# Kernel tuning notes

Hardware: AMD Instinct MI355X
Metric: run time of the kernel (lower is better)

## Reference

```python
import jax, jax.numpy as jnp
import numpy as np

B, S, H, F = 4, 2048, 1024, 4096
E, K = 8, 2


def setup_inputs() -> dict:
    key = jax.random.key(0)
    ks = jax.random.split(key, 8)
    s1 = 1.0 / np.sqrt(H)
    s2 = 1.0 / np.sqrt(F)
    return {
        "hidden_states": jax.random.normal(ks[0], (B, S, H), dtype=jnp.float32),
        "w1": jax.random.normal(ks[1], (E, H, F), dtype=jnp.float32) * s1,
        "b1": jnp.zeros((E, F), dtype=jnp.float32),
        "w2": jax.random.normal(ks[2], (E, F, H), dtype=jnp.float32) * s2,
        "b2": jnp.zeros((E, H), dtype=jnp.float32),
        "router_w": jax.random.normal(ks[3], (H, E), dtype=jnp.float32) * s1,
        "router_b": jnp.zeros((E,), dtype=jnp.float32),
    }


def reference(hidden_states, w1, b1, w2, b2, router_w, router_b):
    b, s, h = hidden_states.shape
    x = hidden_states.reshape(-1, h)              # [T, H]
    # --- router: softmax over expert logits, top-k, renormalize ---
    logits = x @ router_w + router_b              # [T, E]
    probs = jax.nn.softmax(logits, axis=-1)
    top_w, top_i = jax.lax.top_k(probs, K)        # [T, K]
    top_w = top_w / jnp.sum(top_w, axis=-1, keepdims=True)
    # --- dispatch/combine: per-expert FFN, weighted sum (same math as
    # gather/scatter loop in the torch module, expressed densely per expert) ---
    out = jnp.zeros_like(x)
    for e in range(E):
        we = jnp.sum(jnp.where(top_i == e, top_w, 0.0), axis=-1)   # [T]
        he = jax.nn.gelu(x @ w1[e] + b1[e]) @ w2[e] + b2[e]        # [T, H]
        out = out + we[:, None] * he
    return out.reshape(b, s, h)
```

## Files before the change

kernel.cpp:

```cpp
#include <hip/hip_runtime.h>
#include <cstdint>
#include <cstddef>

#define T_TOK 8192
#define HD 1024
#define FD 4096
#define NE 8
#define RCAP 17408

typedef __bf16 bf16_t;
typedef __bf16 bf16x8 __attribute__((ext_vector_type(8)));
typedef __bf16 bf16x4 __attribute__((ext_vector_type(4)));
typedef float floatx4 __attribute__((ext_vector_type(4)));

#define BM 128
#define BN 128
#define BK 64
#define LDS_STRIDE 72

__device__ __forceinline__ float gelu_tanh(float x) {
    float x3 = x * x * x;
    float t = tanhf(0.7978845608028654f * (x + 0.044715f * x3));
    return 0.5f * x * (1.0f + t);
}

__global__ __launch_bounds__(256) void transpose_conv_kernel(
    const float* __restrict__ in, bf16_t* __restrict__ out, int R, int C)
{
    __shared__ float tile[32][33];
    const int e = blockIdx.z;
    const int c0 = blockIdx.x * 32;
    const int r0 = blockIdx.y * 32;
    const float* src = in + (size_t)e * R * C;
    bf16_t* dst = out + (size_t)e * R * C;
    const int tx = threadIdx.x & 31;
    const int ty = threadIdx.x >> 5;
    #pragma unroll
    for (int i = ty; i < 32; i += 8)
        tile[i][tx] = src[(size_t)(r0 + i) * C + c0 + tx];
    __syncthreads();
    #pragma unroll
    for (int i = ty; i < 32; i += 8)
        dst[(size_t)(c0 + i) * R + r0 + tx] = (bf16_t)tile[tx][i];
}

__global__ __launch_bounds__(256) void router_kernel(
    const float* __restrict__ x, const float* __restrict__ rw,
    const float* __restrict__ rb,
    int* __restrict__ tok_e, float* __restrict__ tok_w, int* __restrict__ counts)
{
    const int t = blockIdx.x * 4 + (threadIdx.x >> 6);
    const int lane = threadIdx.x & 63;
    const float* xr = x + (size_t)t * HD;
    float acc[NE];
    #pragma unroll
    for (int e = 0; e < NE; ++e) acc[e] = 0.f;
    #pragma unroll 4
    for (int i = 0; i < HD / 64; ++i) {
        int h = lane + 64 * i;
        float xv = xr[h];
        const float4* w4 = (const float4*)(rw + (size_t)h * NE);
        float4 wa = w4[0], wb = w4[1];
        acc[0] += xv * wa.x; acc[1] += xv * wa.y;
        acc[2] += xv * wa.z; acc[3] += xv * wa.w;
        acc[4] += xv * wb.x; acc[5] += xv * wb.y;
        acc[6] += xv * wb.z; acc[7] += xv * wb.w;
    }
    #pragma unroll
    for (int s = 32; s > 0; s >>= 1)
        #pragma unroll
        for (int e = 0; e < NE; ++e)
            acc[e] += __shfl_xor(acc[e], s, 64);
    if (lane == 0) {
        float l[NE];
        #pragma unroll
        for (int e = 0; e < NE; ++e) l[e] = acc[e] + rb[e];
        int e1 = 0;
        #pragma unroll
        for (int e = 1; e < NE; ++e) if (l[e] > l[e1]) e1 = e;
        int e2 = (e1 == 0) ? 1 : 0;
        #pragma unroll
        for (int e = 0; e < NE; ++e) {
            if (e == e1 || e == e2) continue;
            if (l[e] > l[e2]) e2 = e;
        }
        float m = l[e1];
        float q1 = 1.0f;
        float q2 = expf(l[e2] - m);
        float inv = 1.0f / (q1 + q2);
        tok_e[t * 2]     = e1;
        tok_e[t * 2 + 1] = e2;
        tok_w[t * 2]     = q1 * inv;
        tok_w[t * 2 + 1] = q2 * inv;
        atomicAdd(&counts[e1], 1);
        atomicAdd(&counts[e2], 1);
    }
}

__global__ void offsets_kernel(const int* __restrict__ counts,
                               int* __restrict__ offsets, int* __restrict__ cursors)
{
    if (threadIdx.x == 0) {
        int cum = 0;
        for (int e = 0; e < NE; ++e) {
            offsets[e] = cum;
            cursors[e] = cum;
            cum += (counts[e] + BM - 1) & ~(BM - 1);
        }
    }
}

__global__ __launch_bounds__(256) void gather_kernel(
    const float* __restrict__ x, const int* __restrict__ tok_e,
    const float* __restrict__ tok_w, int* __restrict__ cursors,
    bf16_t* __restrict__ Xg, int* __restrict__ rows_token, float* __restrict__ rows_w)
{
    const int pair = blockIdx.x * 4 + (threadIdx.x >> 6);
    const int lane = threadIdx.x & 63;
    const int t = pair >> 1;
    int pos;
    if (lane == 0) {
        int e = tok_e[pair];
        pos = atomicAdd(&cursors[e], 1);
        rows_token[pos] = t;
        rows_w[pos] = tok_w[pair];
    }
    pos = __shfl(pos, 0, 64);
    const float4* src = (const float4*)(x + (size_t)t * HD);
    bf16_t* dst = Xg + (size_t)pos * HD;
    #pragma unroll
    for (int i = 0; i < HD / 256; ++i) {
        float4 v = src[lane + 64 * i];
        int base = (lane + 64 * i) * 4;
        bf16x4 o;
        o[0] = (bf16_t)v.x; o[1] = (bf16_t)v.y;
        o[2] = (bf16_t)v.z; o[3] = (bf16_t)v.w;
        *(bf16x4*)(dst + base) = o;
    }
}

template<int KDIM>
__device__ __forceinline__ void gemm_tile(
    const bf16_t* __restrict__ aG,
    const bf16_t* __restrict__ bG,
    bf16_t As[BM][LDS_STRIDE], bf16_t Bs[BN][LDS_STRIDE],
    floatx4 acc[4][4])
{
    const int tid = threadIdx.x;
    const int lane = tid & 63;
    const int wave = tid >> 6;
    const int quad = lane >> 4;
    const int l16 = lane & 15;
    const int wm = (wave & 1) * 64;
    const int wn = (wave >> 1) * 64;
    const int r0 = tid >> 3;
    const int c0 = (tid & 7) * 8;

    for (int k0 = 0; k0 < KDIM; k0 += BK) {
        #pragma unroll
        for (int p = 0; p < 4; ++p) {
            int r = p * 32 + r0;
            *(bf16x8*)(&As[r][c0]) = *(const bf16x8*)(aG + (size_t)r * KDIM + k0 + c0);
            *(bf16x8*)(&Bs[r][c0]) = *(const bf16x8*)(bG + (size_t)r * KDIM + k0 + c0);
        }
        __syncthreads();
        #pragma unroll
        for (int kk = 0; kk < BK; kk += 32) {
            bf16x8 af[4], bfr[4];
            #pragma unroll
            for (int i = 0; i < 4; ++i)
                af[i] = *(const bf16x8*)(&As[wm + i * 16 + l16][kk + quad * 8]);
            #pragma unroll
            for (int i = 0; i < 4; ++i)
                bfr[i] = *(const bf16x8*)(&Bs[wn + i * 16 + l16][kk + quad * 8]);
            #pragma unroll
            for (int i = 0; i < 4; ++i)
                #pragma unroll
                for (int j = 0; j < 4; ++j)
                    acc[i][j] = __builtin_amdgcn_mfma_f32_16x16x32_bf16(
                        af[i], bfr[j], acc[i][j], 0, 0, 0);
        }
        __syncthreads();
    }
}

__global__ __launch_bounds__(256) void ffn1_kernel(
    const bf16_t* __restrict__ Xg, const bf16_t* __restrict__ w1t,
    const float* __restrict__ b1, bf16_t* __restrict__ Hb,
    const int* __restrict__ counts, const int* __restrict__ offsets)
{
    const int e = blockIdx.z;
    const int cnt = counts[e];
    const int mtile = blockIdx.y;
    if (mtile * BM >= cnt) return;
    const int m_base = offsets[e] + mtile * BM;
    const int n_base = blockIdx.x * BN;

    __shared__ bf16_t As[BM][LDS_STRIDE];
    __shared__ bf16_t Bs[BN][LDS_STRIDE];
    floatx4 acc[4][4] = {};

    gemm_tile<HD>(Xg + (size_t)m_base * HD,
                  w1t + ((size_t)e * FD + n_base) * HD, As, Bs, acc);

    const int lane = threadIdx.x & 63;
    const int wave = threadIdx.x >> 6;
    const int quad = lane >> 4;
    const int l16 = lane & 15;
    const int wm = (wave & 1) * 64;
    const int wn = (wave >> 1) * 64;
    #pragma unroll
    for (int i = 0; i < 4; ++i) {
        int rl = wm + i * 16 + quad * 4;
        #pragma unroll
        for (int j = 0; j < 4; ++j) {
            int col = n_base + wn + j * 16 + l16;
            float bias = b1[e * FD + col];
            #pragma unroll
            for (int r = 0; r < 4; ++r) {
                float v = acc[i][j][r] + bias;
                Hb[(size_t)(m_base + rl + r) * FD + col] = (bf16_t)gelu_tanh(v);
            }
        }
    }
}

__global__ __launch_bounds__(256) void ffn2_kernel(
    const bf16_t* __restrict__ Hb, const bf16_t* __restrict__ w2t,
    const float* __restrict__ b2, float* __restrict__ out,
    const int* __restrict__ counts, const int* __restrict__ offsets,
    const int* __restrict__ rows_token, const float* __restrict__ rows_w)
{
    const int e = blockIdx.z;
    const int cnt = counts[e];
    const int mtile = blockIdx.y;
    if (mtile * BM >= cnt) return;
    const int m_base = offsets[e] + mtile * BM;
    const int n_base = blockIdx.x * BN;

    __shared__ bf16_t As[BM][LDS_STRIDE];
    __shared__ bf16_t Bs[BN][LDS_STRIDE];
    floatx4 acc[4][4] = {};

    gemm_tile<FD>(Hb + (size_t)m_base * FD,
                  w2t + ((size_t)e * HD + n_base) * FD, As, Bs, acc);

    const int lane = threadIdx.x & 63;
    const int wave = threadIdx.x >> 6;
    const int quad = lane >> 4;
    const int l16 = lane & 15;
    const int wm = (wave & 1) * 64;
    const int wn = (wave >> 1) * 64;
    const int loc_base = mtile * BM;
    #pragma unroll
    for (int i = 0; i < 4; ++i) {
        int rl = wm + i * 16 + quad * 4;
        #pragma unroll
        for (int j = 0; j < 4; ++j) {
            int col = n_base + wn + j * 16 + l16;
            float bias = b2[e * HD + col];
            #pragma unroll
            for (int r = 0; r < 4; ++r) {
                if (loc_base + rl + r < cnt) {
                    int gr = m_base + rl + r;
                    int token = rows_token[gr];
                    float wgt = rows_w[gr];
                    float v = acc[i][j][r] + bias;
                    atomicAdd(&out[(size_t)token * HD + col], wgt * v);
                }
            }
        }
    }
}

extern "C" void kernel_launch(void* const* d_in, const int* in_sizes, int n_in,
                              void* d_out, int out_size, void* d_ws, size_t ws_size,
                              hipStream_t stream)
{
    (void)in_sizes; (void)n_in; (void)ws_size;
    const float* x  = (const float*)d_in[0];
    const float* w1 = (const float*)d_in[1];
    const float* b1 = (const float*)d_in[2];
    const float* w2 = (const float*)d_in[3];
    const float* b2 = (const float*)d_in[4];
    const float* rw = (const float*)d_in[5];
    const float* rb = (const float*)d_in[6];
    float* out = (float*)d_out;

    char* ws = (char*)d_ws;
    size_t off = 0;
    auto alloc = [&](size_t bytes) -> void* {
        void* p = ws + off;
        off = (off + bytes + 255) & ~(size_t)255;
        return p;
    };
    int*    counts     = (int*)alloc(NE * sizeof(int));
    int*    cursors    = (int*)alloc(NE * sizeof(int));
    int*    offsets    = (int*)alloc(NE * sizeof(int));
    int*    tok_e      = (int*)alloc((size_t)T_TOK * 2 * sizeof(int));
    float*  tok_w      = (float*)alloc((size_t)T_TOK * 2 * sizeof(float));
    int*    rows_token = (int*)alloc((size_t)RCAP * sizeof(int));
    float*  rows_w     = (float*)alloc((size_t)RCAP * sizeof(float));
    bf16_t* Xg         = (bf16_t*)alloc((size_t)RCAP * HD * sizeof(bf16_t));
    bf16_t* Hb         = (bf16_t*)alloc((size_t)RCAP * FD * sizeof(bf16_t));
    bf16_t* w1t        = (bf16_t*)alloc((size_t)NE * FD * HD * sizeof(bf16_t));
    bf16_t* w2t        = (bf16_t*)alloc((size_t)NE * HD * FD * sizeof(bf16_t));

    hipMemsetAsync(counts, 0, NE * sizeof(int), stream);
    hipMemsetAsync(out, 0, (size_t)out_size * sizeof(float), stream);

    transpose_conv_kernel<<<dim3(FD / 32, HD / 32, NE), 256, 0, stream>>>(w1, w1t, HD, FD);
    transpose_conv_kernel<<<dim3(HD / 32, FD / 32, NE), 256, 0, stream>>>(w2, w2t, FD, HD);

    router_kernel<<<dim3(T_TOK / 4), 256, 0, stream>>>(x, rw, rb, tok_e, tok_w, counts);

    offsets_kernel<<<dim3(1), 64, 0, stream>>>(counts, offsets, cursors);

    gather_kernel<<<dim3(T_TOK * 2 / 4), 256, 0, stream>>>(
        x, tok_e, tok_w, cursors, Xg, rows_token, rows_w);

    ffn1_kernel<<<dim3(FD / BN, T_TOK / BM, NE), 256, 0, stream>>>(
        Xg, w1t, b1, Hb, counts, offsets);

    ffn2_kernel<<<dim3(HD / BN, T_TOK / BM, NE), 256, 0, stream>>>(
        Hb, w2t, b2, out, counts, offsets, rows_token, rows_w);
}
```

Measured before the change: 1.231 ms.

## Stage GEMM tiles via direct global-to-LDS loads, swizzle workgroups across XCDs

GEMM tile staging now uses global_load_lds so data goes from global memory into LDS without passing through VGPRs, and the LDS tiles lose their row padding. The FFN grids are flattened and remapped so neighbouring tiles land on the same XCD for better L2 reuse. The weight transpose/convert kernel moves to 64x64 tiles with float4 loads and bf16x4 stores. Removing the padding may add LDS bank conflicts on the fragment reads.

```diff
diff --git a/kernel.cpp b/kernel.cpp
--- a/kernel.cpp
+++ b/kernel.cpp
@@ -16,7 +16,6 @@
 #define BM 128
 #define BN 128
 #define BK 64
-#define LDS_STRIDE 72
 
 __device__ __forceinline__ float gelu_tanh(float x) {
     float x3 = x * x * x;
@@ -24,24 +23,47 @@
     return 0.5f * x * (1.0f + t);
 }
 
+__device__ __forceinline__ void stage16(const bf16_t* g, bf16_t* lds_base) {
+    __builtin_amdgcn_global_load_lds(
+        (const __attribute__((address_space(1))) void*)g,
+        (__attribute__((address_space(3))) void*)lds_base,
+        16, 0, 0);
+}
+
 __global__ __launch_bounds__(256) void transpose_conv_kernel(
     const float* __restrict__ in, bf16_t* __restrict__ out, int R, int C)
 {
-    __shared__ float tile[32][33];
+    __shared__ float tile[64][65];
     const int e = blockIdx.z;
-    const int c0 = blockIdx.x * 32;
-    const int r0 = blockIdx.y * 32;
+    const int c0 = blockIdx.x * 64;
+    const int r0 = blockIdx.y * 64;
     const float* src = in + (size_t)e * R * C;
     bf16_t* dst = out + (size_t)e * R * C;
-    const int tx = threadIdx.x & 31;
-    const int ty = threadIdx.x >> 5;
-    #pragma unroll
-    for (int i = ty; i < 32; i += 8)
-        tile[i][tx] = src[(size_t)(r0 + i) * C + c0 + tx];
+
+    const int tc = (threadIdx.x & 15) * 4;
+    const int tr = threadIdx.x >> 4;
+    #pragma unroll
+    for (int p = 0; p < 4; ++p) {
+        int r = tr + p * 16;
+        float4 v = *(const float4*)(src + (size_t)(r0 + r) * C + c0 + tc);
+        tile[r][tc]     = v.x;
+        tile[r][tc + 1] = v.y;
+        tile[r][tc + 2] = v.z;
+        tile[r][tc + 3] = v.w;
+    }
     __syncthreads();
-    #pragma unroll
-    for (int i = ty; i < 32; i += 8)
-        dst[(size_t)(c0 + i) * R + r0 + tx] = (bf16_t)tile[tx][i];
+    const int rw = (threadIdx.x & 15) * 4;
+    const int cw = threadIdx.x >> 4;
+    #pragma unroll
+    for (int p = 0; p < 4; ++p) {
+        int c = cw + p * 16;
+        bf16x4 o;
+        o[0] = (bf16_t)tile[rw][c];
+        o[1] = (bf16_t)tile[rw + 1][c];
+        o[2] = (bf16_t)tile[rw + 2][c];
+        o[3] = (bf16_t)tile[rw + 3][c];
+        *(bf16x4*)(dst + (size_t)(c0 + c) * R + r0 + rw) = o;
+    }
 }
 
 __global__ __launch_bounds__(256) void router_kernel(
@@ -143,7 +165,7 @@
 __device__ __forceinline__ void gemm_tile(
     const bf16_t* __restrict__ aG,
     const bf16_t* __restrict__ bG,
-    bf16_t As[BM][LDS_STRIDE], bf16_t Bs[BN][LDS_STRIDE],
+    bf16_t* __restrict__ As, bf16_t* __restrict__ Bs,
     floatx4 acc[4][4])
 {
     const int tid = threadIdx.x;
@@ -153,15 +175,16 @@
     const int l16 = lane & 15;
     const int wm = (wave & 1) * 64;
     const int wn = (wave >> 1) * 64;
-    const int r0 = tid >> 3;
-    const int c0 = (tid & 7) * 8;
+    const int srow = lane >> 3;
+    const int scol = (lane & 7) * 8;
+    const int wrow = wave * 32;
 
     for (int k0 = 0; k0 < KDIM; k0 += BK) {
         #pragma unroll
         for (int p = 0; p < 4; ++p) {
-            int r = p * 32 + r0;
-            *(bf16x8*)(&As[r][c0]) = *(const bf16x8*)(aG + (size_t)r * KDIM + k0 + c0);
-            *(bf16x8*)(&Bs[r][c0]) = *(const bf16x8*)(bG + (size_t)r * KDIM + k0 + c0);
+            int r = wrow + p * 8;
+            stage16(aG + (size_t)(r + srow) * KDIM + k0 + scol, As + r * BK);
+            stage16(bG + (size_t)(r + srow) * KDIM + k0 + scol, Bs + r * BK);
         }
         __syncthreads();
         #pragma unroll
@@ -169,10 +192,10 @@
             bf16x8 af[4], bfr[4];
             #pragma unroll
             for (int i = 0; i < 4; ++i)
-                af[i] = *(const bf16x8*)(&As[wm + i * 16 + l16][kk + quad * 8]);
+                af[i] = *(const bf16x8*)(As + (wm + i * 16 + l16) * BK + kk + quad * 8);
             #pragma unroll
             for (int i = 0; i < 4; ++i)
-                bfr[i] = *(const bf16x8*)(&Bs[wn + i * 16 + l16][kk + quad * 8]);
+                bfr[i] = *(const bf16x8*)(Bs + (wn + i * 16 + l16) * BK + kk + quad * 8);
             #pragma unroll
             for (int i = 0; i < 4; ++i)
                 #pragma unroll
@@ -184,20 +207,30 @@
     }
 }
 
+__device__ __forceinline__ int xcd_swizzle(int bid, int nwg) {
+    int cpx = nwg >> 3;
+    return (bid & 7) * cpx + (bid >> 3);
+}
+
 __global__ __launch_bounds__(256) void ffn1_kernel(
     const bf16_t* __restrict__ Xg, const bf16_t* __restrict__ w1t,
     const float* __restrict__ b1, bf16_t* __restrict__ Hb,
     const int* __restrict__ counts, const int* __restrict__ offsets)
 {
-    const int e = blockIdx.z;
+    const int nwg = (FD / BN) * (T_TOK / BM) * NE;
+    int wg = xcd_swizzle(blockIdx.x, nwg);
+    const int nt = wg & (FD / BN - 1);
+    int rem = wg >> 5;
+    const int mtile = rem & (T_TOK / BM - 1);
+    const int e = rem >> 6;
+
     const int cnt = counts[e];
-    const int mtile = blockIdx.y;
     if (mtile * BM >= cnt) return;
     const int m_base = offsets[e] + mtile * BM;
-    const int n_base = blockIdx.x * BN;
-
-    __shared__ bf16_t As[BM][LDS_STRIDE];
-    __shared__ bf16_t Bs[BN][LDS_STRIDE];
+    const int n_base = nt * BN;
+
+    __shared__ bf16_t As[BM * BK];
+    __shared__ bf16_t Bs[BN * BK];
     floatx4 acc[4][4] = {};
 
     gemm_tile<HD>(Xg + (size_t)m_base * HD,
@@ -231,15 +264,20 @@
     const int* __restrict__ counts, const int* __restrict__ offsets,
     const int* __restrict__ rows_token, const float* __restrict__ rows_w)
 {
-    const int e = blockIdx.z;
+    const int nwg = (HD / BN) * (T_TOK / BM) * NE;
+    int wg = xcd_swizzle(blockIdx.x, nwg);
+    const int nt = wg & (HD / BN - 1);
+    int rem = wg >> 3;
+    const int mtile = rem & (T_TOK / BM - 1);
+    const int e = rem >> 6;
+
     const int cnt = counts[e];
-    const int mtile = blockIdx.y;
     if (mtile * BM >= cnt) return;
     const int m_base = offsets[e] + mtile * BM;
-    const int n_base = blockIdx.x * BN;
-
-    __shared__ bf16_t As[BM][LDS_STRIDE];
-    __shared__ bf16_t Bs[BN][LDS_STRIDE];
+    const int n_base = nt * BN;
+
+    __shared__ bf16_t As[BM * BK];
+    __shared__ bf16_t Bs[BN * BK];
     floatx4 acc[4][4] = {};
 
     gemm_tile<FD>(Hb + (size_t)m_base * FD,
@@ -309,8 +347,8 @@
     hipMemsetAsync(counts, 0, NE * sizeof(int), stream);
     hipMemsetAsync(out, 0, (size_t)out_size * sizeof(float), stream);
 
-    transpose_conv_kernel<<<dim3(FD / 32, HD / 32, NE), 256, 0, stream>>>(w1, w1t, HD, FD);
-    transpose_conv_kernel<<<dim3(HD / 32, FD / 32, NE), 256, 0, stream>>>(w2, w2t, FD, HD);
+    transpose_conv_kernel<<<dim3(FD / 64, HD / 64, NE), 256, 0, stream>>>(w1, w1t, HD, FD);
+    transpose_conv_kernel<<<dim3(HD / 64, FD / 64, NE), 256, 0, stream>>>(w2, w2t, FD, HD);
 
     router_kernel<<<dim3(T_TOK / 4), 256, 0, stream>>>(x, rw, rb, tok_e, tok_w, counts);
 
@@ -319,9 +357,9 @@
     gather_kernel<<<dim3(T_TOK * 2 / 4), 256, 0, stream>>>(
         x, tok_e, tok_w, cursors, Xg, rows_token, rows_w);
 
-    ffn1_kernel<<<dim3(FD / BN, T_TOK / BM, NE), 256, 0, stream>>>(
+    ffn1_kernel<<<dim3((FD / BN) * (T_TOK / BM) * NE), 256, 0, stream>>>(
         Xg, w1t, b1, Hb, counts, offsets);
 
-    ffn2_kernel<<<dim3(HD / BN, T_TOK / BM, NE), 256, 0, stream>>>(
+    ffn2_kernel<<<dim3((HD / BN) * (T_TOK / BM) * NE), 256, 0, stream>>>(
         Hb, w2t, b2, out, counts, offsets, rows_token, rows_w);
 }
```

New measurement: 1.414 ms. 14.9% more time.
